# Performance work log

Hardware: AMD Instinct MI355X
Metric: run time of the kernel (lower is better)

## Reference

```python
import jax, jax.numpy as jnp
import numpy as np


def setup_inputs() -> dict:
    key = jax.random.key(0)
    k1, k2 = jax.random.split(key)
    BATCH, MOTION_DIM, OUT_DIM = 524288, 20, 512
    input = jax.random.normal(k1, (BATCH, MOTION_DIM), dtype=jnp.float32)
    weight = jax.random.normal(k2, (OUT_DIM, MOTION_DIM), dtype=jnp.float32)
    return {"input": input, "weight": weight}


def reference(input, weight):
    # weight: [512, m]; reduced QR -> Q: [512, m]
    Q, R = jnp.linalg.qr(weight + 1e-08, mode="reduced")
    # Original: sum(diag_embed(input) @ Q.T, dim=1) == input @ Q.T  (same math,
    # the diag-embed matmul just scales row j of Q.T by input[:, j] then sums rows)
    out = jnp.einsum("bm,om->bo", input, Q)  # [batch, 512]
    return out
```

## Files before the change

### kernel.cpp

```cpp
#include <hip/hip_runtime.h>
#include <math.h>

#define MDIM 20
#define ODIM 512
#define LSTR 21
#define ROWS_PER_BLOCK 64

typedef float f4 __attribute__((ext_vector_type(4)));

__global__ __launch_bounds__(256) void qr_kernel(const float* __restrict__ w,
                                                 float* __restrict__ qt) {
  __shared__ float A[ODIM * LSTR];
  __shared__ float tau_s[MDIM];
  __shared__ float wc[MDIM];
  __shared__ float red[4];
  const int tid = threadIdx.x;
  const int lane = tid & 63;
  const int wave = tid >> 6;

  for (int i = tid; i < ODIM * MDIM; i += 256) {
    int r = i / MDIM, c = i - r * MDIM;
    A[r * LSTR + c] = w[i] + 1e-8f;
  }
  __syncthreads();

  for (int j = 0; j < MDIM; ++j) {
    float s = 0.f;
    for (int r = j + 1 + tid; r < ODIM; r += 256) {
      float v = A[r * LSTR + j];
      s += v * v;
    }
    #pragma unroll
    for (int off = 32; off > 0; off >>= 1) s += __shfl_down(s, off, 64);
    if (lane == 0) red[wave] = s;
    __syncthreads();
    float xn2 = red[0] + red[1] + red[2] + red[3];
    float alpha = A[j * LSTR + j];
    float tau, vinv;
    if (xn2 == 0.f) {
      tau = 0.f;
      vinv = 0.f;
    } else {
      float beta = -copysignf(sqrtf(alpha * alpha + xn2), alpha);
      tau = (beta - alpha) / beta;
      vinv = 1.f / (alpha - beta);
    }
    if (tid == 0) tau_s[j] = tau;
    for (int r = j + 1 + tid; r < ODIM; r += 256) A[r * LSTR + j] *= vinv;
    __syncthreads();
    for (int c = j + 1 + wave; c < MDIM; c += 4) {
      float acc = 0.f;
      for (int r = j + 1 + lane; r < ODIM; r += 64)
        acc += A[r * LSTR + j] * A[r * LSTR + c];
      #pragma unroll
      for (int off = 32; off > 0; off >>= 1) acc += __shfl_down(acc, off, 64);
      if (lane == 0) wc[c] = tau * (A[j * LSTR + c] + acc);
    }
    __syncthreads();
    for (int c = j + 1; c < MDIM; ++c) {
      float wcc = wc[c];
      for (int r = j + 1 + tid; r < ODIM; r += 256)
        A[r * LSTR + c] -= A[r * LSTR + j] * wcc;
    }
    __syncthreads();
  }

  for (int i = MDIM - 1; i >= 0; --i) {
    float tau = tau_s[i];
    for (int c = i + 1 + wave; c < MDIM; c += 4) {
      float acc = 0.f;
      for (int r = i + 1 + lane; r < ODIM; r += 64)
        acc += A[r * LSTR + i] * A[r * LSTR + c];
      #pragma unroll
      for (int off = 32; off > 0; off >>= 1) acc += __shfl_down(acc, off, 64);
      if (lane == 0) wc[c] = tau * (A[i * LSTR + c] + acc);
    }
    __syncthreads();
    for (int c = i + 1; c < MDIM; ++c) {
      float wcc = wc[c];
      for (int r = i + tid; r < ODIM; r += 256) {
        float v = (r == i) ? 1.f : A[r * LSTR + i];
        A[r * LSTR + c] -= v * wcc;
      }
    }
    __syncthreads();
    for (int r = tid; r < ODIM; r += 256) {
      float val;
      if (r < i) val = 0.f;
      else if (r == i) val = 1.f - tau;
      else val = -tau * A[r * LSTR + i];
      A[r * LSTR + i] = val;
    }
    __syncthreads();
  }

  for (int idx = tid; idx < MDIM * ODIM; idx += 256) {
    int c = idx >> 9, r = idx & 511;
    qt[idx] = A[r * LSTR + c];
  }
}

__global__ __launch_bounds__(256, 4) void matmul_kernel(
    const float* __restrict__ in, const float* __restrict__ qt,
    float* __restrict__ out, int batch) {
  __shared__ f4 tile4[ROWS_PER_BLOCK * MDIM / 4];
  const int tid = threadIdx.x;
  const int oq = tid & 127;
  const int grp = tid >> 7;
  const int base = blockIdx.x * ROWS_PER_BLOCK;
  int nrows = batch - base;
  if (nrows > ROWS_PER_BLOCK) nrows = ROWS_PER_BLOCK;

  const f4* in4 = (const f4*)(in + (size_t)base * MDIM);
  const int nf4 = nrows * MDIM / 4;
  for (int i = tid; i < nf4; i += 256) tile4[i] = in4[i];

  const f4* qt4 = (const f4*)qt;
  f4 qv[MDIM];
  #pragma unroll
  for (int m = 0; m < MDIM; ++m) qv[m] = qt4[m * 128 + oq];
  __syncthreads();

  f4* out4 = (f4*)out;
  const float* tile = (const float*)tile4;
  #pragma unroll 1
  for (int it = 0; it < ROWS_PER_BLOCK / 2; ++it) {
    const int lr = grp * (ROWS_PER_BLOCK / 2) + it;
    if (lr >= nrows) break;
    const f4* row4 = (const f4*)(tile + lr * MDIM);
    f4 xv[5];
    #pragma unroll
    for (int k = 0; k < 5; ++k) xv[k] = row4[k];
    f4 acc = (f4)(0.f);
    #pragma unroll
    for (int m = 0; m < MDIM; ++m) {
      float x = xv[m / 4][m % 4];
      acc += x * qv[m];
    }
    __builtin_nontemporal_store(acc, &out4[(size_t)(base + lr) * 128 + oq]);
  }
}

extern "C" void kernel_launch(void* const* d_in, const int* in_sizes, int n_in,
                              void* d_out, int out_size, void* d_ws, size_t ws_size,
                              hipStream_t stream) {
  const float* input = (const float*)d_in[0];
  const float* weight = (const float*)d_in[1];
  float* out = (float*)d_out;
  float* qt = (float*)d_ws;
  const int batch = in_sizes[0] / MDIM;

  qr_kernel<<<1, 256, 0, stream>>>(weight, qt);
  const int blocks = (batch + ROWS_PER_BLOCK - 1) / ROWS_PER_BLOCK;
  matmul_kernel<<<blocks, 256, 0, stream>>>(input, qt, out, batch);
}
```

Measured before the change: 1.221 ms.

## Replace Householder QR with Gram-Cholesky plus small QR and triangular inverse

The single-block Householder QR over the 512x20 weight is replaced by an algebraic reformulation. It forms the Gram matrix of rows 20..511 in double, Cholesky-factors it, and stacks that factor under the top 20 rows into a 40x20 matrix for a small Householder QR. It then inverts R and computes Q = W·R^-1. This shrinks the serial single-block setup work, which is tiny next to the large batched matmul. The cost is double-precision arithmetic and possible conditioning and sign differences versus the reference QR.

```diff
diff --git a/kernel.cpp b/kernel.cpp
--- a/kernel.cpp
+++ b/kernel.cpp
@@ -4,99 +4,126 @@
 #define MDIM 20
 #define ODIM 512
 #define LSTR 21
+#define NPAIR 210
 #define ROWS_PER_BLOCK 64
 
 typedef float f4 __attribute__((ext_vector_type(4)));
 
-__global__ __launch_bounds__(256) void qr_kernel(const float* __restrict__ w,
-                                                 float* __restrict__ qt) {
-  __shared__ float A[ODIM * LSTR];
-  __shared__ float tau_s[MDIM];
-  __shared__ float wc[MDIM];
-  __shared__ float red[4];
+__global__ __launch_bounds__(256) void setup_kernel(const float* __restrict__ w,
+                                                    float* __restrict__ qt) {
+  __shared__ float  Ws[ODIM * LSTR];
+  __shared__ double Gd[MDIM * 21];
+  __shared__ double Ad[40 * 21];
+  __shared__ double Rid[MDIM * 21];
+  __shared__ double wcd[MDIM];
+  __shared__ double sc[4];
   const int tid = threadIdx.x;
   const int lane = tid & 63;
   const int wave = tid >> 6;
 
   for (int i = tid; i < ODIM * MDIM; i += 256) {
     int r = i / MDIM, c = i - r * MDIM;
-    A[r * LSTR + c] = w[i] + 1e-8f;
+    Ws[r * LSTR + c] = w[i] + 1e-8f;
+  }
+  __syncthreads();
+
+  if (tid < NPAIR) {
+    int rem = tid, i = 0;
+    while (rem >= MDIM - i) { rem -= MDIM - i; ++i; }
+    const int pi = i, pj = i + rem;
+    double acc = 0.0;
+    for (int r = MDIM; r < ODIM; ++r)
+      acc += (double)Ws[r * LSTR + pi] * (double)Ws[r * LSTR + pj];
+    Gd[pi * 21 + pj] = acc;
+    Gd[pj * 21 + pi] = acc;
+  }
+  __syncthreads();
+
+  for (int k = 0; k < MDIM; ++k) {
+    if (tid == 0) Gd[k * 21 + k] = sqrt(Gd[k * 21 + k]);
+    __syncthreads();
+    if (tid > k && tid < MDIM) Gd[tid * 21 + k] /= Gd[k * 21 + k];
+    __syncthreads();
+    if (tid > k && tid < MDIM) {
+      double ljk = Gd[tid * 21 + k];
+      for (int i = k + 1; i <= tid; ++i) Gd[tid * 21 + i] -= ljk * Gd[i * 21 + k];
+    }
+    __syncthreads();
+  }
+
+  for (int idx = tid; idx < 40 * MDIM; idx += 256) {
+    int r = idx / MDIM, c = idx - r * MDIM;
+    double v;
+    if (r < MDIM) v = (double)Ws[r * LSTR + c];
+    else { int k = r - MDIM; v = (c >= k) ? Gd[c * 21 + k] : 0.0; }
+    Ad[r * 21 + c] = v;
   }
   __syncthreads();
 
   for (int j = 0; j < MDIM; ++j) {
-    float s = 0.f;
-    for (int r = j + 1 + tid; r < ODIM; r += 256) {
-      float v = A[r * LSTR + j];
-      s += v * v;
+    if (tid < 64) {
+      double x = (tid > j && tid < 40) ? Ad[tid * 21 + j] : 0.0;
+      double s = x * x;
+      #pragma unroll
+      for (int off = 32; off > 0; off >>= 1) s += __shfl_down(s, off, 64);
+      if (tid == 0) {
+        double alpha = Ad[j * 21 + j];
+        double beta, tau, vinv;
+        if (s == 0.0) { beta = alpha; tau = 0.0; vinv = 0.0; }
+        else {
+          beta = -copysign(sqrt(alpha * alpha + s), alpha);
+          tau = (beta - alpha) / beta;
+          vinv = 1.0 / (alpha - beta);
+        }
+        sc[0] = tau; sc[1] = vinv; sc[2] = beta;
+      }
     }
-    #pragma unroll
-    for (int off = 32; off > 0; off >>= 1) s += __shfl_down(s, off, 64);
-    if (lane == 0) red[wave] = s;
     __syncthreads();
-    float xn2 = red[0] + red[1] + red[2] + red[3];
-    float alpha = A[j * LSTR + j];
-    float tau, vinv;
-    if (xn2 == 0.f) {
-      tau = 0.f;
-      vinv = 0.f;
-    } else {
-      float beta = -copysignf(sqrtf(alpha * alpha + xn2), alpha);
-      tau = (beta - alpha) / beta;
-      vinv = 1.f / (alpha - beta);
-    }
-    if (tid == 0) tau_s[j] = tau;
-    for (int r = j + 1 + tid; r < ODIM; r += 256) A[r * LSTR + j] *= vinv;
+    const double tau = sc[0], vinv = sc[1];
+    if (tid > j && tid < 40) Ad[tid * 21 + j] *= vinv;
     __syncthreads();
     for (int c = j + 1 + wave; c < MDIM; c += 4) {
-      float acc = 0.f;
-      for (int r = j + 1 + lane; r < ODIM; r += 64)
-        acc += A[r * LSTR + j] * A[r * LSTR + c];
+      double val = 0.0;
+      if (lane == j) val = Ad[j * 21 + c];
+      else if (lane > j && lane < 40) val = Ad[lane * 21 + j] * Ad[lane * 21 + c];
       #pragma unroll
-      for (int off = 32; off > 0; off >>= 1) acc += __shfl_down(acc, off, 64);
-      if (lane == 0) wc[c] = tau * (A[j * LSTR + c] + acc);
+      for (int off = 32; off > 0; off >>= 1) val += __shfl_down(val, off, 64);
+      if (lane == 0) wcd[c] = tau * val;
     }
     __syncthreads();
-    for (int c = j + 1; c < MDIM; ++c) {
-      float wcc = wc[c];
-      for (int r = j + 1 + tid; r < ODIM; r += 256)
-        A[r * LSTR + c] -= A[r * LSTR + j] * wcc;
+    const int ncols = MDIM - 1 - j;
+    if (ncols > 0) {
+      const int total = (40 - j) * ncols;
+      for (int idx = tid; idx < total; idx += 256) {
+        int r = j + idx / ncols, c = j + 1 + idx % ncols;
+        double v = (r == j) ? 1.0 : Ad[r * 21 + j];
+        Ad[r * 21 + c] -= v * wcd[c];
+      }
     }
+    if (tid == 0) Ad[j * 21 + j] = sc[2];
     __syncthreads();
   }
 
-  for (int i = MDIM - 1; i >= 0; --i) {
-    float tau = tau_s[i];
-    for (int c = i + 1 + wave; c < MDIM; c += 4) {
-      float acc = 0.f;
-      for (int r = i + 1 + lane; r < ODIM; r += 64)
-        acc += A[r * LSTR + i] * A[r * LSTR + c];
+  if (tid < MDIM) {
+    const int c = tid;
+    Rid[c * 21 + c] = 1.0 / Ad[c * 21 + c];
+    for (int i = c - 1; i >= 0; --i) {
+      double s = 0.0;
+      for (int k = i + 1; k <= c; ++k) s += Ad[i * 21 + k] * Rid[k * 21 + c];
+      Rid[i * 21 + c] = -s / Ad[i * 21 + i];
+    }
+  }
+  __syncthreads();
+
+  for (int o = tid; o < ODIM; o += 256) {
+    #pragma unroll
+    for (int m = 0; m < MDIM; ++m) {
+      double acc = 0.0;
       #pragma unroll
-      for (int off = 32; off > 0; off >>= 1) acc += __shfl_down(acc, off, 64);
-      if (lane == 0) wc[c] = tau * (A[i * LSTR + c] + acc);
+      for (int k = 0; k <= m; ++k)
+        acc += (double)Ws[o * LSTR + k] * Rid[k * 21 + m];
+      qt[m * ODIM + o] = (float)acc;
     }
-    __syncthreads();
-    for (int c = i + 1; c < MDIM; ++c) {
-      float wcc = wc[c];
-      for (int r = i + tid; r < ODIM; r += 256) {
-        float v = (r == i) ? 1.f : A[r * LSTR + i];
-        A[r * LSTR + c] -= v * wcc;
-      }
-    }
-    __syncthreads();
-    for (int r = tid; r < ODIM; r += 256) {
-      float val;
-      if (r < i) val = 0.f;
-      else if (r == i) val = 1.f - tau;
-      else val = -tau * A[r * LSTR + i];
-      A[r * LSTR + i] = val;
-    }
-    __syncthreads();
-  }
-
-  for (int idx = tid; idx < MDIM * ODIM; idx += 256) {
-    int c = idx >> 9, r = idx & 511;
-    qt[idx] = A[r * LSTR + c];
   }
 }
 
@@ -150,7 +177,7 @@
   float* qt = (float*)d_ws;
   const int batch = in_sizes[0] / MDIM;
 
-  qr_kernel<<<1, 256, 0, stream>>>(weight, qt);
+  setup_kernel<<<1, 256, 0, stream>>>(weight, qt);
   const int blocks = (batch + ROWS_PER_BLOCK - 1) / ROWS_PER_BLOCK;
   matmul_kernel<<<blocks, 256, 0, stream>>>(input, qt, out, batch);
 }
```

After: 1.149 ms. 5.9% less time.
